# Kernel optimization log

Hardware: AMD Instinct MI355X
Metric: run time of the kernel (lower is better)

The kernel has to match this reference:

```python
import jax, jax.numpy as jnp
import numpy as np

NUM_ENTITIES = 100000
NUM_RELATIONS = 8
HIDDEN = 128
N_NODES = 100000
N_EDGES = 500000


def setup_inputs() -> dict:
    key = jax.random.key(0)
    ks = jax.random.split(key, 10)
    scale = 1.0 / np.sqrt(HIDDEN)
    inp = {
        "x_ids": jax.random.randint(ks[0], (N_NODES,), 0, NUM_ENTITIES),
        "edge_index": jax.random.randint(ks[1], (2, N_EDGES), 0, N_NODES),
        "edge_type": jax.random.randint(ks[2], (N_EDGES,), 0, NUM_RELATIONS),
        "emb": jax.random.normal(ks[3], (NUM_ENTITIES, HIDDEN), jnp.float32),
        "W1": jax.random.normal(ks[4], (NUM_RELATIONS, HIDDEN, HIDDEN), jnp.float32) * scale,
        "root1": jax.random.normal(ks[5], (HIDDEN, HIDDEN), jnp.float32) * scale,
        "b1": jnp.zeros((HIDDEN,), jnp.float32),
        "W2": jax.random.normal(ks[6], (NUM_RELATIONS, HIDDEN, HIDDEN), jnp.float32) * scale,
        "root2": jax.random.normal(ks[7], (HIDDEN, HIDDEN), jnp.float32) * scale,
        "b2": jnp.zeros((HIDDEN,), jnp.float32),
    }
    return inp


def rgcn_conv(x, edge_index, edge_type, W, root, bias):
    # x: [N, d]; W: [R, d, d]; PyG RGCNConv with aggr='mean' (per-relation mean)
    N, d = x.shape
    R = W.shape[0]
    src, dst = edge_index[0], edge_index[1]
    # transform every node under every relation: [N, R, d]
    h = jnp.einsum('nd,rdf->nrf', x, W)
    msg = h[src, edge_type]                       # [E, d] gather per edge
    seg = dst * R + edge_type                     # composite (node, relation) segment id
    sums = jax.ops.segment_sum(msg, seg, num_segments=N * R)
    cnt = jax.ops.segment_sum(jnp.ones((msg.shape[0], 1), x.dtype), seg, num_segments=N * R)
    agg = (sums / jnp.maximum(cnt, 1.0)).reshape(N, R, d).sum(axis=1)
    return agg + x @ root + bias


def reference(x_ids, edge_index, edge_type, emb, W1, root1, b1, W2, root2, b2):
    x = emb[x_ids]                                # embedding lookup [N, d]
    x = rgcn_conv(x, edge_index, edge_type, W1, root1, b1)
    x = jax.nn.relu(x)
    x = rgcn_conv(x, edge_index, edge_type, W2, root2, b2)
    return jax.nn.sigmoid(x)
```

## Files before the change

### kernel.cpp

```cpp
#include <hip/hip_runtime.h>

#define HD 128
#define RNUM 8
#define SCAN_BS 2048

typedef __attribute__((ext_vector_type(8))) short short8;
typedef __attribute__((ext_vector_type(4))) float float4e;

__device__ __forceinline__ unsigned short f2bf(float f) {
    unsigned int u = __float_as_uint(f);
    u += 0x7fffu + ((u >> 16) & 1u);
    return (unsigned short)(u >> 16);
}

__device__ __forceinline__ unsigned int pk2(float lo, float hi) {
    return (unsigned int)f2bf(lo) | ((unsigned int)f2bf(hi) << 16);
}

__device__ __forceinline__ void acc2(float4e& a, unsigned int u, int i) {
    a[i]     += __uint_as_float(u << 16);
    a[i + 1] += __uint_as_float(u & 0xffff0000u);
}

__device__ __forceinline__ void gload_lds16(const void* g, void* l) {
    __builtin_amdgcn_global_load_lds(
        (const __attribute__((address_space(1))) void*)g,
        (__attribute__((address_space(3))) void*)l, 16, 0, 0);
}

__global__ void zero_i(int* __restrict__ p, int n) {
    int g = blockIdx.x * blockDim.x + threadIdx.x;
    if (g < n) p[g] = 0;
}

__global__ void prep_kernel(const float* __restrict__ W1, const float* __restrict__ r1,
                            const float* __restrict__ W2, const float* __restrict__ r2,
                            unsigned short* __restrict__ WT,
                            const float* __restrict__ emb, unsigned short* __restrict__ emb16,
                            long long n8) {
    long long g = (long long)blockIdx.x * blockDim.x + threadIdx.x;
    if (g < 18 * 16384) {
        int gi = (int)g;
        int mat = gi >> 14;
        int idx = gi & 16383;
        int d = idx >> 7;
        int f = idx & 127;
        const float* src;
        int m;
        if (mat < 8)       { src = W1; m = mat; }
        else if (mat == 8) { src = r1; m = 0; }
        else if (mat < 17) { src = W2; m = mat - 9; }
        else               { src = r2; m = 0; }
        WT[mat * 16384 + f * 128 + d] = f2bf(src[(size_t)m * 16384 + d * 128 + f]);
    }
    long long h = g - 18 * 16384;
    if (h >= 0 && h < n8) {
        const float4* p = (const float4*)(emb + h * 8);
        float4 v0 = p[0], v1 = p[1];
        uint4 o;
        o.x = pk2(v0.x, v0.y);
        o.y = pk2(v0.z, v0.w);
        o.z = pk2(v1.x, v1.y);
        o.w = pk2(v1.z, v1.w);
        *(uint4*)(emb16 + h * 8) = o;
    }
}

__global__ void count_kernel(const int* __restrict__ ei, const int* __restrict__ et,
                             int* __restrict__ cnt, int E, int N) {
    int e = blockIdx.x * blockDim.x + threadIdx.x;
    if (e < E) atomicAdd(&cnt[ei[E + e] * RNUM + et[e]], 1);
}

__global__ void scan1(const int* __restrict__ in, int* __restrict__ out,
                      int* __restrict__ bsum, int n) {
    __shared__ int s[256];
    const int tid = threadIdx.x;
    const int base = blockIdx.x * SCAN_BS + tid * 8;
    int v[8];
    int sum = 0;
#pragma unroll
    for (int j = 0; j < 8; j++) {
        int x = (base + j < n) ? in[base + j] : 0;
        v[j] = sum;
        sum += x;
    }
    s[tid] = sum;
    __syncthreads();
    for (int off = 1; off < 256; off <<= 1) {
        int tv = (tid >= off) ? s[tid - off] : 0;
        __syncthreads();
        if (tid >= off) s[tid] += tv;
        __syncthreads();
    }
    int excl = (tid > 0) ? s[tid - 1] : 0;
    if (tid == 255) bsum[blockIdx.x] = s[255];
#pragma unroll
    for (int j = 0; j < 8; j++)
        if (base + j < n) out[base + j] = v[j] + excl;
}

__global__ void scan2(int* __restrict__ bsum, int nb) {
    __shared__ int s[512];
    const int tid = threadIdx.x;
    s[tid] = (tid < nb) ? bsum[tid] : 0;
    __syncthreads();
    for (int off = 1; off < 512; off <<= 1) {
        int tv = (tid >= off) ? s[tid - off] : 0;
        __syncthreads();
        if (tid >= off) s[tid] += tv;
        __syncthreads();
    }
    if (tid < nb) bsum[tid] = (tid > 0) ? s[tid - 1] : 0;
}

__global__ void scan3(int* __restrict__ out, int* __restrict__ cur,
                      const int* __restrict__ bsum, int n) {
    const int base = blockIdx.x * SCAN_BS + threadIdx.x * 8;
    const int add = bsum[blockIdx.x];
#pragma unroll
    for (int j = 0; j < 8; j++) {
        int i = base + j;
        if (i < n) {
            int v = out[i] + add;
            out[i] = v;
            cur[i] = v;
        }
    }
}

__global__ void fill_kernel(const int* __restrict__ ei, const int* __restrict__ et,
                            const int* __restrict__ ids,
                            int* __restrict__ cur, int* __restrict__ col,
                            int* __restrict__ colE, int* __restrict__ row_start,
                            int E, int N) {
    int e = blockIdx.x * blockDim.x + threadIdx.x;
    if (e == 0) row_start[RNUM * N] = E;
    if (e < E) {
        int src = ei[e];
        int pos = atomicAdd(&cur[ei[E + e] * RNUM + et[e]], 1);
        col[pos] = src;
        colE[pos] = ids[src];
    }
}

template <bool HAS_IDX, int ACT>
__launch_bounds__(512, 4)
__global__ void rgcn_fused(const int* __restrict__ row_start, const int* __restrict__ col,
                           const int* __restrict__ ids,
                           const unsigned short* __restrict__ x16,
                           const unsigned short* __restrict__ WT,
                           const float* __restrict__ bias,
                           void* __restrict__ CoutV, int N, int E) {
    __shared__ unsigned short As[128 * 128];
    __shared__ unsigned short Ws[128 * 128];

    const int tid = threadIdx.x;
    const int block0 = blockIdx.x * 128;
    const int w = tid >> 6;
    const int lane = tid & 63;
    const int ln15 = lane & 15;
    const int quad = lane >> 4;
    const int rowbase = (w & 1) * 64;
    const int colbase = (w >> 1) * 32;
    const int grp = tid >> 2;
    const int sub4 = tid & 3;
    const int mydst = block0 + grp;
    const bool rowok = (mydst < N);

    float4e acc[4][2];
#pragma unroll
    for (int i = 0; i < 4; i++)
#pragma unroll
        for (int j = 0; j < 2; j++)
#pragma unroll
            for (int q = 0; q < 4; q++) acc[i][j][q] = 0.0f;

#pragma unroll 1
    for (int s = 0; s < RNUM; s++) {
        {
            const unsigned short* Wsrc = WT + s * 16384;
#pragma unroll
            for (int i = 0; i < 4; i++) {
                int c = i * 512 + tid;
                int f = c >> 4;
                int cc = c & 15;
                const void* src = (const void*)(Wsrc + f * 128 + ((cc ^ (f & 15)) << 3));
                int cbase = i * 512 + (tid & ~63);
                gload_lds16(src, (char*)Ws + (size_t)cbase * 16);
            }
        }
        {
            float4e a[8];
#pragma unroll
            for (int j = 0; j < 8; j++) a[j] = (float4e){0.f, 0.f, 0.f, 0.f};
            int s0 = 0, s1 = 0;
            if (rowok) {
                s0 = row_start[mydst * 8 + s];
                s1 = row_start[mydst * 8 + s + 1];
            }
            const float inv = (s1 > s0) ? 1.0f / (float)(s1 - s0) : 0.0f;
#pragma unroll 1
            for (int e = s0; e < s1; e++) {
                int c = col[e];
                const uint4* xp = (const uint4*)(x16 + (size_t)c * HD + sub4 * 32);
                uint4 v0 = xp[0], v1 = xp[1], v2 = xp[2], v3 = xp[3];
                acc2(a[0], v0.x, 0); acc2(a[0], v0.y, 2);
                acc2(a[1], v0.z, 0); acc2(a[1], v0.w, 2);
                acc2(a[2], v1.x, 0); acc2(a[2], v1.y, 2);
                acc2(a[3], v1.z, 0); acc2(a[3], v1.w, 2);
                acc2(a[4], v2.x, 0); acc2(a[4], v2.y, 2);
                acc2(a[5], v2.z, 0); acc2(a[5], v2.w, 2);
                acc2(a[6], v3.x, 0); acc2(a[6], v3.y, 2);
                acc2(a[7], v3.z, 0); acc2(a[7], v3.w, 2);
            }
#pragma unroll
            for (int j = 0; j < 8; j++) a[j] *= inv;
#pragma unroll
            for (int j = 0; j < 4; j++) {
                uint4 o;
                o.x = pk2(a[2 * j][0], a[2 * j][1]);
                o.y = pk2(a[2 * j][2], a[2 * j][3]);
                o.z = pk2(a[2 * j + 1][0], a[2 * j + 1][1]);
                o.w = pk2(a[2 * j + 1][2], a[2 * j + 1][3]);
                int ck = sub4 * 4 + j;
                *(uint4*)&As[grp * 128 + ((ck ^ (grp & 15)) << 3)] = o;
            }
        }
        __syncthreads();

#pragma unroll
        for (int k0 = 0; k0 < 4; k0++) {
            short8 af[4], bf[2];
            const int ck = k0 * 4 + quad;
#pragma unroll
            for (int rt = 0; rt < 4; rt++) {
                int m = rowbase + rt * 16 + ln15;
                af[rt] = *(const short8*)&As[m * 128 + ((ck ^ (m & 15)) << 3)];
            }
#pragma unroll
            for (int ct = 0; ct < 2; ct++) {
                int n = colbase + ct * 16 + ln15;
                bf[ct] = *(const short8*)&Ws[n * 128 + ((ck ^ (n & 15)) << 3)];
            }
#pragma unroll
            for (int rt = 0; rt < 4; rt++)
#pragma unroll
                for (int ct = 0; ct < 2; ct++)
                    acc[rt][ct] = __builtin_amdgcn_mfma_f32_16x16x32_bf16(
                        af[rt], bf[ct], acc[rt][ct], 0, 0, 0);
        }
        __syncthreads();
    }

    {
        const unsigned short* Wsrc = WT + RNUM * 16384;
#pragma unroll
        for (int i = 0; i < 4; i++) {
            int c = i * 512 + tid;
            int f = c >> 4;
            int cc = c & 15;
            const void* src = (const void*)(Wsrc + f * 128 + ((cc ^ (f & 15)) << 3));
            int cbase = i * 512 + (tid & ~63);
            gload_lds16(src, (char*)Ws + (size_t)cbase * 16);
        }
        uint4 o0 = {0u, 0u, 0u, 0u}, o1 = o0, o2 = o0, o3 = o0;
        if (rowok) {
            int srcn = HAS_IDX ? ids[mydst] : mydst;
            const uint4* xp = (const uint4*)(x16 + (size_t)srcn * HD + sub4 * 32);
            o0 = xp[0]; o1 = xp[1]; o2 = xp[2]; o3 = xp[3];
        }
        const int ck0 = sub4 * 4;
        *(uint4*)&As[grp * 128 + (((ck0 + 0) ^ (grp & 15)) << 3)] = o0;
        *(uint4*)&As[grp * 128 + (((ck0 + 1) ^ (grp & 15)) << 3)] = o1;
        *(uint4*)&As[grp * 128 + (((ck0 + 2) ^ (grp & 15)) << 3)] = o2;
        *(uint4*)&As[grp * 128 + (((ck0 + 3) ^ (grp & 15)) << 3)] = o3;
        __syncthreads();
#pragma unroll
        for (int k0 = 0; k0 < 4; k0++) {
            short8 af[4], bf[2];
            const int ck = k0 * 4 + quad;
#pragma unroll
            for (int rt = 0; rt < 4; rt++) {
                int m = rowbase + rt * 16 + ln15;
                af[rt] = *(const short8*)&As[m * 128 + ((ck ^ (m & 15)) << 3)];
            }
#pragma unroll
            for (int ct = 0; ct < 2; ct++) {
                int n = colbase + ct * 16 + ln15;
                bf[ct] = *(const short8*)&Ws[n * 128 + ((ck ^ (n & 15)) << 3)];
            }
#pragma unroll
            for (int rt = 0; rt < 4; rt++)
#pragma unroll
                for (int ct = 0; ct < 2; ct++)
                    acc[rt][ct] = __builtin_amdgcn_mfma_f32_16x16x32_bf16(
                        af[rt], bf[ct], acc[rt][ct], 0, 0, 0);
        }
        __syncthreads();
    }

#pragma unroll
    for (int ct = 0; ct < 2; ct++) {
        int ncol = colbase + ct * 16 + ln15;
        float bv = bias[ncol];
#pragma unroll
        for (int rt = 0; rt < 4; rt++) {
#pragma unroll
            for (int rg = 0; rg < 4; rg++) {
                int rowg = block0 + rowbase + rt * 16 + quad * 4 + rg;
                if (rowg < N) {
                    float v = acc[rt][ct][rg] + bv;
                    if (ACT == 0) {
                        v = fmaxf(v, 0.0f);
                        ((unsigned short*)CoutV)[(size_t)rowg * HD + ncol] = f2bf(v);
                    } else {
                        v = 1.0f / (1.0f + expf(-v));
                        ((float*)CoutV)[(size_t)rowg * HD + ncol] = v;
                    }
                }
            }
        }
    }
}

extern "C" void kernel_launch(void* const* d_in, const int* in_sizes, int n_in,
                              void* d_out, int out_size, void* d_ws, size_t ws_size,
                              hipStream_t stream) {
    const int*   x_ids = (const int*)d_in[0];
    const int*   ei    = (const int*)d_in[1];
    const int*   et    = (const int*)d_in[2];
    const float* emb   = (const float*)d_in[3];
    const float* W1    = (const float*)d_in[4];
    const float* root1 = (const float*)d_in[5];
    const float* b1    = (const float*)d_in[6];
    const float* W2    = (const float*)d_in[7];
    const float* root2 = (const float*)d_in[8];
    const float* b2    = (const float*)d_in[9];

    const int N = in_sizes[0];
    const int E = in_sizes[1] / 2;
    const int NS = RNUM * N;
    const long long embElems = (long long)in_sizes[3];
    float* out = (float*)d_out;

    char* ws = (char*)d_ws;
    size_t off = 0;
    int* row_start = (int*)(ws + off); off += (size_t)(NS + 4) * 4;
    int* col       = (int*)(ws + off); off += (size_t)E * 4;
    int* colE      = (int*)(ws + off); off += (size_t)E * 4;
    int* bsum      = (int*)(ws + off); off += 4096;
    unsigned short* WT    = (unsigned short*)(ws + off); off += (size_t)18 * 16384 * 2;
    unsigned short* emb16 = (unsigned short*)(ws + off); off += (size_t)embElems * 2;
    unsigned short* z16   = (unsigned short*)(ws + off); off += (size_t)N * HD * 2;
    int* cur = (int*)z16;

    const int scanBlocks = (NS + SCAN_BS - 1) / SCAN_BS;
    const int layerGrid = (N + 127) / 128;

    zero_i<<<(NS + 255) / 256, 256, 0, stream>>>(cur, NS);
    count_kernel<<<(E + 255) / 256, 256, 0, stream>>>(ei, et, cur, E, N);
    scan1<<<scanBlocks, 256, 0, stream>>>(cur, row_start, bsum, NS);
    scan2<<<1, 512, 0, stream>>>(bsum, scanBlocks);
    scan3<<<scanBlocks, 256, 0, stream>>>(row_start, cur, bsum, NS);
    fill_kernel<<<(E + 255) / 256, 256, 0, stream>>>(ei, et, x_ids, cur, col, colE,
                                                     row_start, E, N);

    {
        long long n8 = embElems / 8;
        long long total = 18 * 16384 + n8;
        prep_kernel<<<(unsigned int)((total + 255) / 256), 256, 0, stream>>>(
            W1, root1, W2, root2, WT, emb, emb16, n8);
    }

    rgcn_fused<true, 0><<<layerGrid, 512, 0, stream>>>(
        row_start, colE, x_ids, emb16, WT, b1, (void*)z16, N, E);
    rgcn_fused<false, 1><<<layerGrid, 512, 0, stream>>>(
        row_start, col, nullptr, z16, WT + 9 * 16384, b2, (void*)out, N, E);
}
```

Measured before the change: 409.1 us.

## Use persistent atomic tile scheduler, register-resident weights, and software-pipelined gathers

Turns the fused RGCN layer kernel into a persistent kernel capped at 512 blocks. Each block pulls 128-row tiles from a global atomic counter, which prep_kernel resets. Weight fragments now go straight from global memory into registers instead of being staged through LDS, which halves shared memory use and can raise occupancy. The neighbor gather loop prefetches the next row before accumulating the current one. In exchange it adds per-tile atomics and barriers, and every wave does redundant global weight loads, which lean on L2.

Result: slower. 440.8 us (+7.7%).

```diff
diff --git a/kernel.cpp b/kernel.cpp
--- a/kernel.cpp
+++ b/kernel.cpp
@@ -22,12 +22,6 @@
     a[i + 1] += __uint_as_float(u & 0xffff0000u);
 }
 
-__device__ __forceinline__ void gload_lds16(const void* g, void* l) {
-    __builtin_amdgcn_global_load_lds(
-        (const __attribute__((address_space(1))) void*)g,
-        (__attribute__((address_space(3))) void*)l, 16, 0, 0);
-}
-
 __global__ void zero_i(int* __restrict__ p, int n) {
     int g = blockIdx.x * blockDim.x + threadIdx.x;
     if (g < n) p[g] = 0;
@@ -37,8 +31,9 @@
                             const float* __restrict__ W2, const float* __restrict__ r2,
                             unsigned short* __restrict__ WT,
                             const float* __restrict__ emb, unsigned short* __restrict__ emb16,
-                            long long n8) {
+                            int* __restrict__ tctr, long long n8) {
     long long g = (long long)blockIdx.x * blockDim.x + threadIdx.x;
+    if (g == 0) { tctr[0] = 0; tctr[1] = 0; }
     if (g < 18 * 16384) {
         int gi = (int)g;
         int mat = gi >> 14;
@@ -151,12 +146,12 @@
                            const unsigned short* __restrict__ x16,
                            const unsigned short* __restrict__ WT,
                            const float* __restrict__ bias,
+                           int* __restrict__ tctr, int numTiles,
                            void* __restrict__ CoutV, int N, int E) {
     __shared__ unsigned short As[128 * 128];
-    __shared__ unsigned short Ws[128 * 128];
+    __shared__ int tileShare;
 
     const int tid = threadIdx.x;
-    const int block0 = blockIdx.x * 128;
     const int w = tid >> 6;
     const int lane = tid & 63;
     const int ln15 = lane & 15;
@@ -165,158 +160,138 @@
     const int colbase = (w >> 1) * 32;
     const int grp = tid >> 2;
     const int sub4 = tid & 3;
-    const int mydst = block0 + grp;
-    const bool rowok = (mydst < N);
-
-    float4e acc[4][2];
-#pragma unroll
-    for (int i = 0; i < 4; i++)
-#pragma unroll
-        for (int j = 0; j < 2; j++)
-#pragma unroll
-            for (int q = 0; q < 4; q++) acc[i][j][q] = 0.0f;
+
+    for (;;) {
+        if (tid == 0) tileShare = atomicAdd(tctr, 1);
+        __syncthreads();
+        const int tile = tileShare;
+        if (tile >= numTiles) break;
+        const int block0 = tile * 128;
+        const int mydst = block0 + grp;
+        const bool rowok = (mydst < N);
+
+        float4e acc[4][2];
+#pragma unroll
+        for (int i = 0; i < 4; i++)
+#pragma unroll
+            for (int j = 0; j < 2; j++)
+#pragma unroll
+                for (int q = 0; q < 4; q++) acc[i][j][q] = 0.0f;
 
 #pragma unroll 1
-    for (int s = 0; s < RNUM; s++) {
-        {
-            const unsigned short* Wsrc = WT + s * 16384;
-#pragma unroll
-            for (int i = 0; i < 4; i++) {
-                int c = i * 512 + tid;
-                int f = c >> 4;
-                int cc = c & 15;
-                const void* src = (const void*)(Wsrc + f * 128 + ((cc ^ (f & 15)) << 3));
-                int cbase = i * 512 + (tid & ~63);
-                gload_lds16(src, (char*)Ws + (size_t)cbase * 16);
+        for (int s = 0; s < RNUM + 1; s++) {
+            if (s < RNUM) {
+                float4e a[8];
+#pragma unroll
+                for (int j = 0; j < 8; j++) a[j] = (float4e){0.f, 0.f, 0.f, 0.f};
+                int s0 = 0, s1 = 0;
+                if (rowok) {
+                    s0 = row_start[mydst * 8 + s];
+                    s1 = row_start[mydst * 8 + s + 1];
+                }
+                const float inv = (s1 > s0) ? 1.0f / (float)(s1 - s0) : 0.0f;
+                if (s1 > s0) {
+                    const uint4* xp = (const uint4*)(x16 + (size_t)col[s0] * HD + sub4 * 32);
+                    uint4 w0 = xp[0], w1 = xp[1], w2 = xp[2], w3 = xp[3];
+#pragma unroll 1
+                    for (int e = s0 + 1; e < s1; e++) {
+                        const uint4* xq = (const uint4*)(x16 + (size_t)col[e] * HD + sub4 * 32);
+                        uint4 n0 = xq[0], n1 = xq[1], n2 = xq[2], n3 = xq[3];
+                        acc2(a[0], w0.x, 0); acc2(a[0], w0.y, 2);
+                        acc2(a[1], w0.z, 0); acc2(a[1], w0.w, 2);
+                        acc2(a[2], w1.x, 0); acc2(a[2], w1.y, 2);
+                        acc2(a[3], w1.z, 0); acc2(a[3], w1.w, 2);
+                        acc2(a[4], w2.x, 0); acc2(a[4], w2.y, 2);
+                        acc2(a[5], w2.z, 0); acc2(a[5], w2.w, 2);
+                        acc2(a[6], w3.x, 0); acc2(a[6], w3.y, 2);
+                        acc2(a[7], w3.z, 0); acc2(a[7], w3.w, 2);
+                        w0 = n0; w1 = n1; w2 = n2; w3 = n3;
+                    }
+                    acc2(a[0], w0.x, 0); acc2(a[0], w0.y, 2);
+                    acc2(a[1], w0.z, 0); acc2(a[1], w0.w, 2);
+                    acc2(a[2], w1.x, 0); acc2(a[2], w1.y, 2);
+                    acc2(a[3], w1.z, 0); acc2(a[3], w1.w, 2);
+                    acc2(a[4], w2.x, 0); acc2(a[4], w2.y, 2);
+                    acc2(a[5], w2.z, 0); acc2(a[5], w2.w, 2);
+                    acc2(a[6], w3.x, 0); acc2(a[6], w3.y, 2);
+                    acc2(a[7], w3.z, 0); acc2(a[7], w3.w, 2);
+                }
+#pragma unroll
+                for (int j = 0; j < 8; j++) a[j] *= inv;
+#pragma unroll
+                for (int j = 0; j < 4; j++) {
+                    uint4 o;
+                    o.x = pk2(a[2 * j][0], a[2 * j][1]);
+                    o.y = pk2(a[2 * j][2], a[2 * j][3]);
+                    o.z = pk2(a[2 * j + 1][0], a[2 * j + 1][1]);
+                    o.w = pk2(a[2 * j + 1][2], a[2 * j + 1][3]);
+                    int ck = sub4 * 4 + j;
+                    *(uint4*)&As[grp * 128 + ((ck ^ (grp & 15)) << 3)] = o;
+                }
+            } else {
+                uint4 o0 = {0u, 0u, 0u, 0u}, o1 = o0, o2 = o0, o3 = o0;
+                if (rowok) {
+                    int srcn = HAS_IDX ? ids[mydst] : mydst;
+                    const uint4* xp = (const uint4*)(x16 + (size_t)srcn * HD + sub4 * 32);
+                    o0 = xp[0]; o1 = xp[1]; o2 = xp[2]; o3 = xp[3];
+                }
+                const int ck0 = sub4 * 4;
+                *(uint4*)&As[grp * 128 + (((ck0 + 0) ^ (grp & 15)) << 3)] = o0;
+                *(uint4*)&As[grp * 128 + (((ck0 + 1) ^ (grp & 15)) << 3)] = o1;
+                *(uint4*)&As[grp * 128 + (((ck0 + 2) ^ (grp & 15)) << 3)] = o2;
+                *(uint4*)&As[grp * 128 + (((ck0 + 3) ^ (grp & 15)) << 3)] = o3;
             }
+
+            short8 breg[2][4];
+            {
+                const unsigned short* Wb = WT + s * 16384;
+#pragma unroll
+                for (int ct = 0; ct < 2; ct++) {
+                    const unsigned short* wn = Wb + (colbase + ct * 16 + ln15) * 128 + quad * 8;
+#pragma unroll
+                    for (int k0 = 0; k0 < 4; k0++)
+                        breg[ct][k0] = *(const short8*)(wn + k0 * 32);
+                }
+            }
+            __syncthreads();
+
+#pragma unroll
+            for (int k0 = 0; k0 < 4; k0++) {
+                short8 af[4];
+                const int ck = k0 * 4 + quad;
+#pragma unroll
+                for (int rt = 0; rt < 4; rt++) {
+                    int m = rowbase + rt * 16 + ln15;
+                    af[rt] = *(const short8*)&As[m * 128 + ((ck ^ (m & 15)) << 3)];
+                }
+#pragma unroll
+                for (int rt = 0; rt < 4; rt++)
+#pragma unroll
+                    for (int ct = 0; ct < 2; ct++)
+                        acc[rt][ct] = __builtin_amdgcn_mfma_f32_16x16x32_bf16(
+                            af[rt], breg[ct][k0], acc[rt][ct], 0, 0, 0);
+            }
+            __syncthreads();
         }
-        {
-            float4e a[8];
-#pragma unroll
-            for (int j = 0; j < 8; j++) a[j] = (float4e){0.f, 0.f, 0.f, 0.f};
-            int s0 = 0, s1 = 0;
-            if (rowok) {
-                s0 = row_start[mydst * 8 + s];
-                s1 = row_start[mydst * 8 + s + 1];
-            }
-            const float inv = (s1 > s0) ? 1.0f / (float)(s1 - s0) : 0.0f;
-#pragma unroll 1
-            for (int e = s0; e < s1; e++) {
-                int c = col[e];
-                const uint4* xp = (const uint4*)(x16 + (size_t)c * HD + sub4 * 32);
-                uint4 v0 = xp[0], v1 = xp[1], v2 = xp[2], v3 = xp[3];
-                acc2(a[0], v0.x, 0); acc2(a[0], v0.y, 2);
-                acc2(a[1], v0.z, 0); acc2(a[1], v0.w, 2);
-                acc2(a[2], v1.x, 0); acc2(a[2], v1.y, 2);
-                acc2(a[3], v1.z, 0); acc2(a[3], v1.w, 2);
-                acc2(a[4], v2.x, 0); acc2(a[4], v2.y, 2);
-                acc2(a[5], v2.z, 0); acc2(a[5], v2.w, 2);
-                acc2(a[6], v3.x, 0); acc2(a[6], v3.y, 2);
-                acc2(a[7], v3.z, 0); acc2(a[7], v3.w, 2);
-            }
-#pragma unroll
-            for (int j = 0; j < 8; j++) a[j] *= inv;
-#pragma unroll
-            for (int j = 0; j < 4; j++) {
-                uint4 o;
-                o.x = pk2(a[2 * j][0], a[2 * j][1]);
-                o.y = pk2(a[2 * j][2], a[2 * j][3]);
-                o.z = pk2(a[2 * j + 1][0], a[2 * j + 1][1]);
-                o.w = pk2(a[2 * j + 1][2], a[2 * j + 1][3]);
-                int ck = sub4 * 4 + j;
-                *(uint4*)&As[grp * 128 + ((ck ^ (grp & 15)) << 3)] = o;
-            }
-        }
-        __syncthreads();
-
-#pragma unroll
-        for (int k0 = 0; k0 < 4; k0++) {
-            short8 af[4], bf[2];
-            const int ck = k0 * 4 + quad;
+
+#pragma unroll
+        for (int ct = 0; ct < 2; ct++) {
+            int ncol = colbase + ct * 16 + ln15;
+            float bv = bias[ncol];
 #pragma unroll
             for (int rt = 0; rt < 4; rt++) {
-                int m = rowbase + rt * 16 + ln15;
-                af[rt] = *(const short8*)&As[m * 128 + ((ck ^ (m & 15)) << 3)];
-            }
-#pragma unroll
-            for (int ct = 0; ct < 2; ct++) {
-                int n = colbase + ct * 16 + ln15;
-                bf[ct] = *(const short8*)&Ws[n * 128 + ((ck ^ (n & 15)) << 3)];
-            }
-#pragma unroll
-            for (int rt = 0; rt < 4; rt++)
-#pragma unroll
-                for (int ct = 0; ct < 2; ct++)
-                    acc[rt][ct] = __builtin_amdgcn_mfma_f32_16x16x32_bf16(
-                        af[rt], bf[ct], acc[rt][ct], 0, 0, 0);
-        }
-        __syncthreads();
-    }
-
-    {
-        const unsigned short* Wsrc = WT + RNUM * 16384;
-#pragma unroll
-        for (int i = 0; i < 4; i++) {
-            int c = i * 512 + tid;
-            int f = c >> 4;
-            int cc = c & 15;
-            const void* src = (const void*)(Wsrc + f * 128 + ((cc ^ (f & 15)) << 3));
-            int cbase = i * 512 + (tid & ~63);
-            gload_lds16(src, (char*)Ws + (size_t)cbase * 16);
-        }
-        uint4 o0 = {0u, 0u, 0u, 0u}, o1 = o0, o2 = o0, o3 = o0;
-        if (rowok) {
-            int srcn = HAS_IDX ? ids[mydst] : mydst;
-            const uint4* xp = (const uint4*)(x16 + (size_t)srcn * HD + sub4 * 32);
-            o0 = xp[0]; o1 = xp[1]; o2 = xp[2]; o3 = xp[3];
-        }
-        const int ck0 = sub4 * 4;
-        *(uint4*)&As[grp * 128 + (((ck0 + 0) ^ (grp & 15)) << 3)] = o0;
-        *(uint4*)&As[grp * 128 + (((ck0 + 1) ^ (grp & 15)) << 3)] = o1;
-        *(uint4*)&As[grp * 128 + (((ck0 + 2) ^ (grp & 15)) << 3)] = o2;
-        *(uint4*)&As[grp * 128 + (((ck0 + 3) ^ (grp & 15)) << 3)] = o3;
-        __syncthreads();
-#pragma unroll
-        for (int k0 = 0; k0 < 4; k0++) {
-            short8 af[4], bf[2];
-            const int ck = k0 * 4 + quad;
-#pragma unroll
-            for (int rt = 0; rt < 4; rt++) {
-                int m = rowbase + rt * 16 + ln15;
-                af[rt] = *(const short8*)&As[m * 128 + ((ck ^ (m & 15)) << 3)];
-            }
-#pragma unroll
-            for (int ct = 0; ct < 2; ct++) {
-                int n = colbase + ct * 16 + ln15;
-                bf[ct] = *(const short8*)&Ws[n * 128 + ((ck ^ (n & 15)) << 3)];
-            }
-#pragma unroll
-            for (int rt = 0; rt < 4; rt++)
-#pragma unroll
-                for (int ct = 0; ct < 2; ct++)
-                    acc[rt][ct] = __builtin_amdgcn_mfma_f32_16x16x32_bf16(
-                        af[rt], bf[ct], acc[rt][ct], 0, 0, 0);
-        }
-        __syncthreads();
-    }
-
-#pragma unroll
-    for (int ct = 0; ct < 2; ct++) {
-        int ncol = colbase + ct * 16 + ln15;
-        float bv = bias[ncol];
-#pragma unroll
-        for (int rt = 0; rt < 4; rt++) {
-#pragma unroll
-            for (int rg = 0; rg < 4; rg++) {
-                int rowg = block0 + rowbase + rt * 16 + quad * 4 + rg;
-                if (rowg < N) {
-                    float v = acc[rt][ct][rg] + bv;
-                    if (ACT == 0) {
-                        v = fmaxf(v, 0.0f);
-                        ((unsigned short*)CoutV)[(size_t)rowg * HD + ncol] = f2bf(v);
-                    } else {
-                        v = 1.0f / (1.0f + expf(-v));
-                        ((float*)CoutV)[(size_t)rowg * HD + ncol] = v;
+#pragma unroll
+                for (int rg = 0; rg < 4; rg++) {
+                    int rowg = block0 + rowbase + rt * 16 + quad * 4 + rg;
+                    if (rowg < N) {
+                        float v = acc[rt][ct][rg] + bv;
+                        if (ACT == 0) {
+                            v = fmaxf(v, 0.0f);
+                            ((unsigned short*)CoutV)[(size_t)rowg * HD + ncol] = f2bf(v);
+                        } else {
+                            v = 1.0f / (1.0f + expf(-v));
+                            ((float*)CoutV)[(size_t)rowg * HD + ncol] = v;
+                        }
                     }
                 }
             }
@@ -353,10 +328,12 @@
     unsigned short* WT    = (unsigned short*)(ws + off); off += (size_t)18 * 16384 * 2;
     unsigned short* emb16 = (unsigned short*)(ws + off); off += (size_t)embElems * 2;
     unsigned short* z16   = (unsigned short*)(ws + off); off += (size_t)N * HD * 2;
-    int* cur = (int*)z16;
+    int* cur  = (int*)z16;
+    int* tctr = bsum + 1000;
 
     const int scanBlocks = (NS + SCAN_BS - 1) / SCAN_BS;
-    const int layerGrid = (N + 127) / 128;
+    const int numTiles = (N + 127) / 128;
+    const int layerGrid = (numTiles < 512) ? numTiles : 512;
 
     zero_i<<<(NS + 255) / 256, 256, 0, stream>>>(cur, NS);
     count_kernel<<<(E + 255) / 256, 256, 0, stream>>>(ei, et, cur, E, N);
@@ -370,11 +347,11 @@
         long long n8 = embElems / 8;
         long long total = 18 * 16384 + n8;
         prep_kernel<<<(unsigned int)((total + 255) / 256), 256, 0, stream>>>(
-            W1, root1, W2, root2, WT, emb, emb16, n8);
+            W1, root1, W2, root2, WT, emb, emb16, tctr, n8);
     }
 
     rgcn_fused<true, 0><<<layerGrid, 512, 0, stream>>>(
-        row_start, colE, x_ids, emb16, WT, b1, (void*)z16, N, E);
+        row_start, colE, x_ids, emb16, WT, b1, tctr, numTiles, (void*)z16, N, E);
     rgcn_fused<false, 1><<<layerGrid, 512, 0, stream>>>(
-        row_start, col, nullptr, z16, WT + 9 * 16384, b2, (void*)out, N, E);
-}
+        row_start, col, nullptr, z16, WT + 9 * 16384, b2, tctr + 1, numTiles, (void*)out, N, E);
+}
```
